# Kernel optimization log

Hardware: AMD Instinct MI355X
Metric: run time of the kernel (lower is better)

Reference implementation:

```python
import jax, jax.numpy as jnp
import numpy as np

NUM_TABLES = 26
VOCAB = 100000
D = 128          # sparse_feature_size == mlp_bot[-1]
B = 8192
P = 10           # fixed pooling factor per bag
DENSE = 13
BOT = [512, 256, 128]
TOP = [1024, 1024, 512, 256, 1]
NF = NUM_TABLES + 1  # features entering dot interaction


def setup_inputs() -> dict:
    key = jax.random.key(0)
    ks = iter(jax.random.split(key, 32))
    inp = {}
    inp["dense_x"] = jax.random.normal(next(ks), (B, DENSE), dtype=jnp.float32)
    inp["sparse_indices"] = jax.random.randint(next(ks), (NUM_TABLES, B * P), 0, VOCAB, dtype=jnp.int32)
    # EmbeddingBag weights init: uniform(-0.01, 0.01)
    inp["emb_tables"] = jax.random.uniform(next(ks), (NUM_TABLES, VOCAB, D), jnp.float32, -0.01, 0.01)
    def xavier(k, shape):
        fan_out, fan_in = shape
        lim = np.sqrt(6.0 / (fan_in + fan_out)).astype(np.float32)
        return jax.random.uniform(k, shape, jnp.float32, -lim, lim)
    dims_bot = [DENSE] + BOT
    for i in range(len(BOT)):
        inp[f"bot_w{i}"] = xavier(next(ks), (dims_bot[i + 1], dims_bot[i]))
        inp[f"bot_b{i}"] = jnp.zeros((dims_bot[i + 1],), jnp.float32)
    interact_dim = NF * (NF - 1) // 2 + BOT[-1]  # 351 + 128 = 479
    dims_top = [interact_dim] + TOP
    for i in range(len(TOP)):
        inp[f"top_w{i}"] = xavier(next(ks), (dims_top[i + 1], dims_top[i]))
        inp[f"top_b{i}"] = jnp.zeros((dims_top[i + 1],), jnp.float32)
    return inp


def reference(dense_x, sparse_indices, emb_tables,
              bot_w0, bot_b0, bot_w1, bot_b1, bot_w2, bot_b2,
              top_w0, top_b0, top_w1, top_b1, top_w2, top_b2,
              top_w3, top_b3, top_w4, top_b4):
    # bottom MLP (Linear + ReLU on every layer)
    x = dense_x
    for w, b in ((bot_w0, bot_b0), (bot_w1, bot_b1), (bot_w2, bot_b2)):
        x = jax.nn.relu(x @ w.T + b)  # [B, 128]

    # multi-table EmbeddingBag sum pooling (fixed pooling factor P)
    idx = sparse_indices.reshape(NUM_TABLES, B, P)
    ly = jax.vmap(lambda tab, i: tab[i].sum(axis=1))(emb_tables, idx)  # [T, B, D]

    # dot interaction: bmm + upper-triangular gather
    T_feat = jnp.concatenate([x[None], ly], axis=0).transpose(1, 0, 2)  # [B, NF, D]
    Z = jnp.einsum('bnd,bmd->bnm', T_feat, T_feat)                       # [B, NF, NF]
    li, lj = np.triu_indices(NF, k=1)
    Zflat = Z[:, li, lj]                                                 # [B, NF*(NF-1)/2]
    z = jnp.concatenate([x, Zflat], axis=1)                              # [B, 479]

    # top MLP: ReLU on all but last layer
    h = z
    tops = ((top_w0, top_b0), (top_w1, top_b1), (top_w2, top_b2), (top_w3, top_b3))
    for w, b in tops:
        h = jax.nn.relu(h @ w.T + b)
    p = h @ top_w4.T + top_b4  # [B, 1]
    return jax.nn.sigmoid(p.squeeze(1))
```

## Files before the change

### kernel.cpp

```cpp
#include <hip/hip_runtime.h>
#include <hip/hip_bf16.h>
#include <cstdint>

typedef __attribute__((ext_vector_type(8))) short bf16x8;
typedef __attribute__((ext_vector_type(4))) short bf16x4;
typedef __attribute__((ext_vector_type(4))) float f32x4;

#define B_SZ 8192
#define TROW 3456

__device__ __forceinline__ void gld_lds16(const void* g, void* l) {
    __builtin_amdgcn_global_load_lds(
        (const __attribute__((address_space(1))) unsigned int*)g,
        (__attribute__((address_space(3))) unsigned int*)l, 16, 0, 0);
}

__device__ __forceinline__ short f2bf_bits(float v) {
    return __builtin_bit_cast(short, __float2bfloat16(v));
}

struct CvtJob { const float* in; __hip_bfloat16* out; int N, K, Kp; };
struct CvtJobs { CvtJob j[6]; int start[7]; };

__device__ __forceinline__ void cvt_dev8(int lb, int tid, const CvtJobs& J) {
    int chunk = lb * 256 + tid;
    int e = chunk * 8;
    if (e >= J.start[6]) return;
    int k = 0;
    #pragma unroll
    for (int i = 1; i < 6; i++) if (e >= J.start[i]) k = i;
    const CvtJob& job = J.j[k];
    int local = e - J.start[k];
    float v[8];
    if (job.K == job.Kp) {
        const float4* p = (const float4*)(job.in + local);
        float4 a = p[0], b = p[1];
        v[0]=a.x; v[1]=a.y; v[2]=a.z; v[3]=a.w; v[4]=b.x; v[5]=b.y; v[6]=b.z; v[7]=b.w;
    } else {
        int n = local / job.Kp, kk = local - n * job.Kp;
        #pragma unroll
        for (int i = 0; i < 8; i++)
            v[i] = (kk + i < job.K) ? job.in[(size_t)n * job.K + kk + i] : 0.f;
    }
    bf16x8 o;
    #pragma unroll
    for (int i = 0; i < 8; i++)
        o[i] = f2bf_bits(v[i]);
    *(bf16x8*)(job.out + local) = o;
}

__device__ __forceinline__ void bot0_dev(int lb, int tid, const float* __restrict__ x,
    const float* __restrict__ w, const float* __restrict__ bias,
    __hip_bfloat16* __restrict__ o, float* xs) {
    int m0 = lb * 4;
    if (tid < 52) xs[tid] = x[(size_t)m0 * 13 + tid];
    __syncthreads();
    for (int c = tid; c < 512; c += 256) {
        const float* wr = w + (size_t)c * 13;
        float bv = bias[c];
        #pragma unroll
        for (int r = 0; r < 4; r++) {
            float s = bv;
            #pragma unroll
            for (int k = 0; k < 13; k++) s += xs[r * 13 + k] * wr[k];
            o[(size_t)(m0 + r) * 512 + c] = __float2bfloat16(fmaxf(s, 0.f));
        }
    }
}

__global__ __launch_bounds__(256) void k_pre(CvtJobs J, int cvtB,
    const float* dx, const float* w0, const float* b0, __hip_bfloat16* bufA) {
    __shared__ float xs[64];
    int blk = blockIdx.x, tid = threadIdx.x;
    if (blk < cvtB) { cvt_dev8(blk, tid, J); return; }
    bot0_dev(blk - cvtB, tid, dx, w0, b0, bufA, xs);
}

__global__ __launch_bounds__(256) void emb_kernel(const int* __restrict__ idx,
                                                  const float* __restrict__ tab,
                                                  __hip_bfloat16* __restrict__ T) {
    int lane = threadIdx.x & 63, wv = threadIdx.x >> 6;
    int p = blockIdx.x * 4 + wv;
    int t = p >> 13;
    int b = p & 8191;
    const int* ip = idx + (size_t)t * 81920 + b * 10;
    const float* tb = tab + (size_t)t * 100000 * 128;
    int half = lane >> 5, l32 = lane & 31;
    float4 s = {0.f, 0.f, 0.f, 0.f};
    #pragma unroll
    for (int j = 0; j < 10; j += 2) {
        int r = ip[j + half];
        float4 v = ((const float4*)(tb + (size_t)r * 128))[l32];
        s.x += v.x; s.y += v.y; s.z += v.z; s.w += v.w;
    }
    s.x += __shfl_xor(s.x, 32, 64);
    s.y += __shfl_xor(s.y, 32, 64);
    s.z += __shfl_xor(s.z, 32, 64);
    s.w += __shfl_xor(s.w, 32, 64);
    if (half == 0) {
        bf16x4 o;
        o[0] = f2bf_bits(s.x); o[1] = f2bf_bits(s.y);
        o[2] = f2bf_bits(s.z); o[3] = f2bf_bits(s.w);
        ((bf16x4*)(T + (size_t)b * TROW + (1 + t) * 128))[l32] = o;
    }
}

template<int TM, int TN, int WM, int WN>
__global__ __launch_bounds__(256) void gemm_t(const __hip_bfloat16* __restrict__ A,
                                              const __hip_bfloat16* __restrict__ W,
                                              const float* __restrict__ bias,
                                              __hip_bfloat16* __restrict__ C,
                                              int M, int N, int K, int ldc) {
    constexpr int ROWS = TM + TN;
    constexpr int CH = ROWS * 4 / 256;
    constexpr int MI = TM / WM / 16;
    constexpr int NI = TN / WN / 16;
    __shared__ __align__(16) __hip_bfloat16 ABs[ROWS * 32];

    const int tid = threadIdx.x;
    const int lane = tid & 63, wave = tid >> 6;
    const int wmI = wave / WN, wnI = wave % WN;
    const int m0 = blockIdx.y * TM, n0 = blockIdx.x * TN;

    const __hip_bfloat16* gp[CH];
    #pragma unroll
    for (int c = 0; c < CH; c++) {
        int gid = c * 256 + tid;
        int row = gid >> 2, col = (gid & 3) * 8;
        gp[c] = (row < TM ? A + (size_t)(m0 + row) * K
                          : W + (size_t)(n0 + row - TM) * K) + col;
    }

    f32x4 acc[MI][NI] = {};
    const int fr = lane & 15, fkb = (lane >> 4) * 8;

    for (int k0 = 0; k0 < K; k0 += 32) {
        __syncthreads();
        #pragma unroll
        for (int c = 0; c < CH; c++)
            gld_lds16(gp[c] + k0, &ABs[(c * 256 + wave * 64) * 8]);
        asm volatile("s_waitcnt vmcnt(0)" ::: "memory");
        __syncthreads();
        bf16x8 a[MI], b[NI];
        #pragma unroll
        for (int i = 0; i < MI; i++)
            a[i] = *(const bf16x8*)&ABs[(wmI * (TM / WM) + i * 16 + fr) * 32 + fkb];
        #pragma unroll
        for (int j = 0; j < NI; j++)
            b[j] = *(const bf16x8*)&ABs[(TM + wnI * (TN / WN) + j * 16 + fr) * 32 + fkb];
        #pragma unroll
        for (int i = 0; i < MI; i++)
            #pragma unroll
            for (int j = 0; j < NI; j++)
                acc[i][j] = __builtin_amdgcn_mfma_f32_16x16x32_bf16(a[i], b[j], acc[i][j], 0, 0, 0);
    }

    const int fq = lane >> 4;
    #pragma unroll
    for (int i = 0; i < MI; i++) {
        #pragma unroll
        for (int j = 0; j < NI; j++) {
            int n = n0 + wnI * (TN / WN) + j * 16 + fr;
            float bv = bias[n];
            #pragma unroll
            for (int r = 0; r < 4; r++) {
                int m = m0 + wmI * (TM / WM) + i * 16 + fq * 4 + r;
                C[(size_t)m * ldc + n] = __float2bfloat16(fmaxf(acc[i][j][r] + bv, 0.f));
            }
        }
    }
}

__global__ __launch_bounds__(256) void k_int(const __hip_bfloat16* __restrict__ T,
                                             __hip_bfloat16* __restrict__ z) {
    int lane = threadIdx.x & 63, wave = threadIdx.x >> 6;
    int b = blockIdx.x * 4 + wave;
    const __hip_bfloat16* Tb = T + (size_t)b * TROW;

    const int fr = lane & 15, fkb = (lane >> 4) * 8;
    bf16x8 fr2[2][4];
    #pragma unroll
    for (int mi = 0; mi < 2; mi++)
        #pragma unroll
        for (int kt = 0; kt < 4; kt++)
            fr2[mi][kt] = *(const bf16x8*)&Tb[(mi * 16 + fr) * 128 + kt * 32 + fkb];

    f32x4 acc[2][2] = {};
    #pragma unroll
    for (int kt = 0; kt < 4; kt++)
        #pragma unroll
        for (int mi = 0; mi < 2; mi++)
            #pragma unroll
            for (int ni = 0; ni < 2; ni++)
                acc[mi][ni] = __builtin_amdgcn_mfma_f32_16x16x32_bf16(fr2[mi][kt], fr2[ni][kt], acc[mi][ni], 0, 0, 0);

    __hip_bfloat16* zb = z + (size_t)b * 512;
    ((unsigned*)zb)[lane] = ((const unsigned*)Tb)[lane];
    if (lane < 33) zb[479 + lane] = __float2bfloat16(0.f);
    const int fq = lane >> 4;
    #pragma unroll
    for (int mi = 0; mi < 2; mi++)
        #pragma unroll
        for (int ni = 0; ni < 2; ni++)
            #pragma unroll
            for (int r = 0; r < 4; r++) {
                int m = mi * 16 + fq * 4 + r;
                int n = ni * 16 + fr;
                if (m < 27 && n < 27 && m < n) {
                    int p = m * 26 - (m * (m - 1)) / 2 + (n - m - 1);
                    zb[128 + p] = __float2bfloat16(acc[mi][ni][r]);
                }
            }
}

__global__ __launch_bounds__(256) void final_kernel(const __hip_bfloat16* __restrict__ h,
                                                    const float* __restrict__ w,
                                                    const float* __restrict__ bias,
                                                    float* __restrict__ out) {
    int lane = threadIdx.x & 63, wv = threadIdx.x >> 6;
    int s = blockIdx.x * 4 + wv;
    const __hip_bfloat16* hp = h + (size_t)s * 256;
    float sum = 0.f;
    #pragma unroll
    for (int i = 0; i < 4; i++) {
        int k = i * 64 + lane;
        sum += __bfloat162float(hp[k]) * w[k];
    }
    #pragma unroll
    for (int off = 32; off; off >>= 1) sum += __shfl_down(sum, off, 64);
    if (lane == 0) out[s] = 1.f / (1.f + expf(-(sum + bias[0])));
}

extern "C" void kernel_launch(void* const* d_in, const int* in_sizes, int n_in,
                              void* d_out, int out_size, void* d_ws, size_t ws_size,
                              hipStream_t stream) {
    const float* dense_x = (const float*)d_in[0];
    const int* sidx      = (const int*)d_in[1];
    const float* emb     = (const float*)d_in[2];
    const float* bw0 = (const float*)d_in[3];  const float* bb0 = (const float*)d_in[4];
    const float* bw1 = (const float*)d_in[5];  const float* bb1 = (const float*)d_in[6];
    const float* bw2 = (const float*)d_in[7];  const float* bb2 = (const float*)d_in[8];
    const float* tw0 = (const float*)d_in[9];  const float* tb0 = (const float*)d_in[10];
    const float* tw1 = (const float*)d_in[11]; const float* tb1 = (const float*)d_in[12];
    const float* tw2 = (const float*)d_in[13]; const float* tb2 = (const float*)d_in[14];
    const float* tw3 = (const float*)d_in[15]; const float* tb3 = (const float*)d_in[16];
    const float* tw4 = (const float*)d_in[17]; const float* tb4 = (const float*)d_in[18];
    float* out = (float*)d_out;

    char* ws = (char*)d_ws;
    size_t off = 0;
    auto alloc = [&](size_t bytes) {
        off = (off + 255) & ~(size_t)255;
        void* p = ws + off;
        off += bytes;
        return p;
    };
    __hip_bfloat16* Wb1 = (__hip_bfloat16*)alloc((size_t)256 * 512 * 2);
    __hip_bfloat16* Wb2 = (__hip_bfloat16*)alloc((size_t)128 * 256 * 2);
    __hip_bfloat16* Wt0 = (__hip_bfloat16*)alloc((size_t)1024 * 512 * 2);
    __hip_bfloat16* Wt1 = (__hip_bfloat16*)alloc((size_t)1024 * 1024 * 2);
    __hip_bfloat16* Wt2 = (__hip_bfloat16*)alloc((size_t)512 * 1024 * 2);
    __hip_bfloat16* Wt3 = (__hip_bfloat16*)alloc((size_t)256 * 512 * 2);
    __hip_bfloat16* bufA = (__hip_bfloat16*)alloc((size_t)B_SZ * 512 * 2);
    __hip_bfloat16* bufB = (__hip_bfloat16*)alloc((size_t)B_SZ * 256 * 2);
    __hip_bfloat16* Tbuf = (__hip_bfloat16*)alloc((size_t)B_SZ * TROW * 2);
    __hip_bfloat16* zbuf = (__hip_bfloat16*)alloc((size_t)B_SZ * 512 * 2);
    __hip_bfloat16* h0   = (__hip_bfloat16*)alloc((size_t)B_SZ * 1024 * 2);
    __hip_bfloat16* h1   = (__hip_bfloat16*)alloc((size_t)B_SZ * 1024 * 2);
    __hip_bfloat16* h2   = (__hip_bfloat16*)alloc((size_t)B_SZ * 512 * 2);
    __hip_bfloat16* h3   = (__hip_bfloat16*)alloc((size_t)B_SZ * 256 * 2);

    CvtJobs J;
    auto setJob = [&](int i, const float* in, __hip_bfloat16* o, int N, int K, int Kp) {
        J.j[i] = {in, o, N, K, Kp};
    };
    setJob(0, bw1, Wb1, 256, 512, 512);
    setJob(1, bw2, Wb2, 128, 256, 256);
    setJob(2, tw0, Wt0, 1024, 479, 512);
    setJob(3, tw1, Wt1, 1024, 1024, 1024);
    setJob(4, tw2, Wt2, 512, 1024, 1024);
    setJob(5, tw3, Wt3, 256, 512, 512);
    J.start[0] = 0;
    for (int i = 0; i < 6; i++) J.start[i + 1] = J.start[i] + J.j[i].N * J.j[i].Kp;
    const int cvtB = (J.start[6] / 8 + 255) / 256;

    k_pre<<<cvtB + B_SZ / 4, 256, 0, stream>>>(J, cvtB, dense_x, bw0, bb0, bufA);

    emb_kernel<<<26 * B_SZ / 4, 256, 0, stream>>>(sidx, emb, Tbuf);

    gemm_t<128, 64, 2, 2><<<dim3(256 / 64, B_SZ / 128), 256, 0, stream>>>(bufA, Wb1, bb1, bufB, B_SZ, 256, 512, 256);
    gemm_t< 64, 64, 2, 2><<<dim3(128 / 64, B_SZ /  64), 256, 0, stream>>>(bufB, Wb2, bb2, Tbuf, B_SZ, 128, 256, TROW);

    k_int<<<B_SZ / 4, 256, 0, stream>>>(Tbuf, zbuf);

    gemm_t<128,128, 2, 2><<<dim3(1024 /128, B_SZ / 128), 256, 0, stream>>>(zbuf, Wt0, tb0, h0, B_SZ, 1024, 512, 1024);
    gemm_t<128,128, 2, 2><<<dim3(1024 /128, B_SZ / 128), 256, 0, stream>>>(h0, Wt1, tb1, h1, B_SZ, 1024, 1024, 1024);
    gemm_t<128,128, 2, 2><<<dim3( 512 /128, B_SZ / 128), 256, 0, stream>>>(h1, Wt2, tb2, h2, B_SZ, 512, 1024, 512);
    gemm_t<128, 64, 2, 2><<<dim3( 256 / 64, B_SZ / 128), 256, 0, stream>>>(h2, Wt3, tb3, h3, B_SZ, 256, 512, 256);

    final_kernel<<<B_SZ / 4, 256, 0, stream>>>(h3, tw4, tb4, out);
}
```

Before: 327.8 us.

## Split embedding gather across pre and bottom-GEMM kernels, add tile swizzle

The embedding-bag gather is split in two halves of 13 tables each. The first half runs in the same launch as weight conversion and the first bottom layer, and the second half runs in the same launch as the second bottom GEMM. This lets the memory-bound gather overlap compute-bound work and removes separate launches. GEMMs now use a 1D grid with a tile swizzle that remaps tile IDs so consecutive blocks spread across 8 groups, likely intended to improve cache locality across XCDs. Mixing heterogeneous blocks in one grid can cause load imbalance, and the fused kernel's LDS footprint is sized for the GEMM path.

Result: faster. 312.2 us (-4.8%).

```diff
diff --git a/kernel.cpp b/kernel.cpp
--- a/kernel.cpp
+++ b/kernel.cpp
@@ -68,20 +68,12 @@
     }
 }
 
-__global__ __launch_bounds__(256) void k_pre(CvtJobs J, int cvtB,
-    const float* dx, const float* w0, const float* b0, __hip_bfloat16* bufA) {
-    __shared__ float xs[64];
-    int blk = blockIdx.x, tid = threadIdx.x;
-    if (blk < cvtB) { cvt_dev8(blk, tid, J); return; }
-    bot0_dev(blk - cvtB, tid, dx, w0, b0, bufA, xs);
-}
-
-__global__ __launch_bounds__(256) void emb_kernel(const int* __restrict__ idx,
-                                                  const float* __restrict__ tab,
-                                                  __hip_bfloat16* __restrict__ T) {
-    int lane = threadIdx.x & 63, wv = threadIdx.x >> 6;
-    int p = blockIdx.x * 4 + wv;
-    int t = p >> 13;
+__device__ __forceinline__ void emb_dev(int lb, int tid, int t0,
+    const int* __restrict__ idx, const float* __restrict__ tab,
+    __hip_bfloat16* __restrict__ T) {
+    int lane = tid & 63, wv = tid >> 6;
+    int p = lb * 4 + wv;
+    int t = t0 + (p >> 13);
     int b = p & 8191;
     const int* ip = idx + (size_t)t * 81920 + b * 10;
     const float* tb = tab + (size_t)t * 100000 * 128;
@@ -106,21 +98,25 @@
 }
 
 template<int TM, int TN, int WM, int WN>
-__global__ __launch_bounds__(256) void gemm_t(const __hip_bfloat16* __restrict__ A,
-                                              const __hip_bfloat16* __restrict__ W,
-                                              const float* __restrict__ bias,
-                                              __hip_bfloat16* __restrict__ C,
-                                              int M, int N, int K, int ldc) {
+__device__ __forceinline__ void gemm_dev(int tileId, int nTiles, int nbx, int tid,
+    const __hip_bfloat16* __restrict__ A, const __hip_bfloat16* __restrict__ W,
+    const float* __restrict__ bias, __hip_bfloat16* __restrict__ C,
+    int K, int ldc, __hip_bfloat16* ABs) {
     constexpr int ROWS = TM + TN;
     constexpr int CH = ROWS * 4 / 256;
     constexpr int MI = TM / WM / 16;
     constexpr int NI = TN / WN / 16;
-    __shared__ __align__(16) __hip_bfloat16 ABs[ROWS * 32];
-
-    const int tid = threadIdx.x;
+
+    int swz = tileId;
+    if ((nTiles & 7) == 0) {
+        int q = nTiles >> 3;
+        swz = (tileId & 7) * q + (tileId >> 3);
+    }
+    const int by = swz / nbx, bx = swz - by * nbx;
+    const int m0 = by * TM, n0 = bx * TN;
+
     const int lane = tid & 63, wave = tid >> 6;
     const int wmI = wave / WN, wnI = wave % WN;
-    const int m0 = blockIdx.y * TM, n0 = blockIdx.x * TN;
 
     const __hip_bfloat16* gp[CH];
     #pragma unroll
@@ -169,6 +165,35 @@
             }
         }
     }
+}
+
+template<int TM, int TN, int WM, int WN>
+__global__ __launch_bounds__(256) void gemm_k(const __hip_bfloat16* A, const __hip_bfloat16* W,
+                                              const float* bias, __hip_bfloat16* C,
+                                              int nbx, int K, int ldc) {
+    __shared__ __align__(16) __hip_bfloat16 ABs[(TM + TN) * 32];
+    gemm_dev<TM, TN, WM, WN>(blockIdx.x, gridDim.x, nbx, threadIdx.x, A, W, bias, C, K, ldc, ABs);
+}
+
+__global__ __launch_bounds__(256) void k_pre_emb(CvtJobs J, int cvtB,
+    const float* dx, const float* w0, const float* b0, __hip_bfloat16* bufA,
+    int t0, const int* sidx, const float* tab, __hip_bfloat16* T) {
+    __shared__ float xs[64];
+    int blk = blockIdx.x, tid = threadIdx.x;
+    if (blk < cvtB) { cvt_dev8(blk, tid, J); return; }
+    blk -= cvtB;
+    if (blk < B_SZ / 4) { bot0_dev(blk, tid, dx, w0, b0, bufA, xs); return; }
+    emb_dev(blk - B_SZ / 4, tid, t0, sidx, tab, T);
+}
+
+__global__ __launch_bounds__(256) void k_gemm_emb(const __hip_bfloat16* A, const __hip_bfloat16* W,
+    const float* bias, __hip_bfloat16* C, int nbx, int K, int ldc, int gB,
+    int t0, const int* sidx, const float* tab, __hip_bfloat16* T) {
+    __shared__ __align__(16) __hip_bfloat16 ABs[(128 + 64) * 32];
+    if (blockIdx.x < gB)
+        gemm_dev<128, 64, 2, 2>(blockIdx.x, gB, nbx, threadIdx.x, A, W, bias, C, K, ldc, ABs);
+    else
+        emb_dev(blockIdx.x - gB, threadIdx.x, t0, sidx, tab, T);
 }
 
 __global__ __launch_bounds__(256) void k_int(const __hip_bfloat16* __restrict__ T,
@@ -284,19 +309,20 @@
     for (int i = 0; i < 6; i++) J.start[i + 1] = J.start[i] + J.j[i].N * J.j[i].Kp;
     const int cvtB = (J.start[6] / 8 + 255) / 256;
 
-    k_pre<<<cvtB + B_SZ / 4, 256, 0, stream>>>(J, cvtB, dense_x, bw0, bb0, bufA);
-
-    emb_kernel<<<26 * B_SZ / 4, 256, 0, stream>>>(sidx, emb, Tbuf);
-
-    gemm_t<128, 64, 2, 2><<<dim3(256 / 64, B_SZ / 128), 256, 0, stream>>>(bufA, Wb1, bb1, bufB, B_SZ, 256, 512, 256);
-    gemm_t< 64, 64, 2, 2><<<dim3(128 / 64, B_SZ /  64), 256, 0, stream>>>(bufB, Wb2, bb2, Tbuf, B_SZ, 128, 256, TROW);
+    k_pre_emb<<<cvtB + B_SZ / 4 + 13 * B_SZ / 4, 256, 0, stream>>>(
+        J, cvtB, dense_x, bw0, bb0, bufA, 0, sidx, emb, Tbuf);
+
+    k_gemm_emb<<<256 + 13 * B_SZ / 4, 256, 0, stream>>>(
+        bufA, Wb1, bb1, bufB, 256 / 64, 512, 256, 256, 13, sidx, emb, Tbuf);
+
+    gemm_k< 64, 64, 2, 2><<<(B_SZ / 64) * (128 / 64), 256, 0, stream>>>(bufB, Wb2, bb2, Tbuf, 128 / 64, 256, TROW);
 
     k_int<<<B_SZ / 4, 256, 0, stream>>>(Tbuf, zbuf);
 
-    gemm_t<128,128, 2, 2><<<dim3(1024 /128, B_SZ / 128), 256, 0, stream>>>(zbuf, Wt0, tb0, h0, B_SZ, 1024, 512, 1024);
-    gemm_t<128,128, 2, 2><<<dim3(1024 /128, B_SZ / 128), 256, 0, stream>>>(h0, Wt1, tb1, h1, B_SZ, 1024, 1024, 1024);
-    gemm_t<128,128, 2, 2><<<dim3( 512 /128, B_SZ / 128), 256, 0, stream>>>(h1, Wt2, tb2, h2, B_SZ, 512, 1024, 512);
-    gemm_t<128, 64, 2, 2><<<dim3( 256 / 64, B_SZ / 128), 256, 0, stream>>>(h2, Wt3, tb3, h3, B_SZ, 256, 512, 256);
+    gemm_k<128,128, 2, 2><<<(B_SZ / 128) * (1024 / 128), 256, 0, stream>>>(zbuf, Wt0, tb0, h0, 1024 / 128, 512, 1024);
+    gemm_k<128,128, 2, 2><<<(B_SZ / 128) * (1024 / 128), 256, 0, stream>>>(h0, Wt1, tb1, h1, 1024 / 128, 1024, 1024);
+    gemm_k<128,128, 2, 2><<<(B_SZ / 128) * ( 512 / 128), 256, 0, stream>>>(h1, Wt2, tb2, h2, 512 / 128, 1024, 512);
+    gemm_k<128, 64, 2, 2><<<(B_SZ / 128) * ( 256 /  64), 256, 0, stream>>>(h2, Wt3, tb3, h3, 256 / 64, 512, 256);
 
     final_kernel<<<B_SZ / 4, 256, 0, stream>>>(h3, tw4, tb4, out);
 }
```
